# Optimization experiments

Hardware: AMD Instinct MI355X
Metric: run time of the kernel (lower is better)

Reference implementation:

```python
import jax, jax.numpy as jnp
import numpy as np

B, L, D_IN = 2, 4096, 512
H, D_K, D_V, D_OUT = 8, 64, 64, 512


def setup_inputs() -> dict:
    key = jax.random.key(0)
    k0, k1, k2, k3, k4 = jax.random.split(key, 5)
    x = jax.random.normal(k0, (B, L, D_IN), dtype=jnp.float32)
    W_q = jax.random.uniform(k1, (H, D_IN, D_K), dtype=jnp.float32)
    W_k = jax.random.uniform(k2, (H, D_IN, D_K), dtype=jnp.float32)
    W_v = jax.random.uniform(k3, (H, D_IN, D_V), dtype=jnp.float32)
    W_o = jax.random.uniform(k4, (H, D_V, D_OUT), dtype=jnp.float32)
    return {"x": x, "W_q": W_q, "W_k": W_k, "W_v": W_v, "W_o": W_o}


def reference(x, W_q, W_k, W_v, W_o):
    # x: (b, l, d_in); projections per head -> (b, h, l, d)
    Q = jnp.einsum('hjk,blj->bhlk', W_q, x)
    K = jnp.einsum('hjk,blj->bhlk', W_k, x)
    V = jnp.einsum('hjv,blj->bhlv', W_v, x)
    # no softmax: pure bilinear attention (Q K^T) V
    scores = jnp.einsum('bhik,bhjk->bhij', Q, K)          # (b, h, l, l)
    values = jnp.einsum('bhqk,bhkv->bhqv', scores, V)     # (b, h, l, d_v)
    return jnp.einsum('hvo,bhlv->blo', W_o, values)       # (b, l, d_out)
```

## Files before the change

kernel.cpp:

```cpp
#include <hip/hip_runtime.h>
#include <cstdint>


#define BDIM 2
#define LDIM 4096
#define DIN 512
#define HDIM 8
#define DK 64
#define DV 64
#define DOUT 512
#define NXTX 256
#define NMID 128
#define SMEM_MAIN 34816

using bf16_t = __bf16;
typedef __bf16 bf16x8 __attribute__((ext_vector_type(8)));
typedef float floatx4 __attribute__((ext_vector_type(4)));

constexpr size_t OFF_XB  = 4096;
constexpr size_t OFF_XT  = OFF_XB  + (size_t)BDIM * LDIM * DIN * 2;
constexpr size_t OFF_WQT = OFF_XT  + (size_t)BDIM * LDIM * DIN * 2;
constexpr size_t OFF_WKT = OFF_WQT + (size_t)HDIM * DK * DIN * 2;
constexpr size_t OFF_WVT = OFF_WKT + (size_t)HDIM * DK * DIN * 2;
constexpr size_t OFF_WOT = OFF_WVT + (size_t)HDIM * DV * DIN * 2;
constexpr size_t OFF_QP  = OFF_WOT + (size_t)HDIM * DOUT * DV * 2;
constexpr size_t OFF_G32 = OFF_QP  + (size_t)BDIM * LDIM * DIN * 2;
constexpr size_t OFF_MP  = OFF_G32 + (size_t)BDIM * DIN * DIN * 4;

__device__ __forceinline__ unsigned short f2bf(float f) {
    unsigned int u = __builtin_bit_cast(unsigned int, f);
    u += 0x7FFFu + ((u >> 16) & 1u);
    return (unsigned short)(u >> 16);
}

__device__ __forceinline__ float bf2f(unsigned short u) {
    unsigned int v = ((unsigned int)u) << 16;
    return __builtin_bit_cast(float, v);
}

__device__ __forceinline__ void gld_lds16(const void* g, void* l) {
    __builtin_amdgcn_global_load_lds(
        (const __attribute__((address_space(1))) void*)g,
        (__attribute__((address_space(3))) void*)l, 16, 0, 0);
}

template <int BM, int BN, int BK, int OUT_MODE>
__device__ __forceinline__ void gemm_tn(char* smem, const bf16_t* A,
                                        const bf16_t* B, void* Cp, int K,
                                        int lda, int ldb, int ldc, int tm,
                                        int tn) {
    constexpr int WM = BM / 2, WN = BN / 2;
    constexpr int FM = WM / 16, FN = WN / 16;
    constexpr int CPR = BK / 8;
    bf16_t* As = (bf16_t*)smem;
    bf16_t* Bs = As + BM * BK;
    const int tid = threadIdx.x;
    const int lane = tid & 63;
    const int wr = (tid >> 7) & 1;
    const int wc = (tid >> 6) & 1;

    A += (size_t)tm * lda;
    B += (size_t)tn * ldb;

    floatx4 acc[FM][FN] = {};

    for (int k0 = 0; k0 < K; k0 += BK) {
#pragma unroll
        for (int i = 0; i < (BM * CPR) / 256; ++i) {
            int c = i * 256 + tid;
            int m = c / CPR, kc = c % CPR;
            gld_lds16(A + (size_t)m * lda + k0 + kc * 8, As + c * 8);
        }
#pragma unroll
        for (int i = 0; i < (BN * CPR) / 256; ++i) {
            int c = i * 256 + tid;
            int m = c / CPR, kc = c % CPR;
            gld_lds16(B + (size_t)m * ldb + k0 + kc * 8, Bs + c * 8);
        }
        __syncthreads();

#pragma unroll
        for (int kk = 0; kk < BK; kk += 32) {
            bf16x8 aF[FM], bF[FN];
#pragma unroll
            for (int fm = 0; fm < FM; ++fm)
                aF[fm] = *(const bf16x8*)(As + (wr * WM + fm * 16 + (lane & 15)) * BK +
                                          kk + (lane >> 4) * 8);
#pragma unroll
            for (int fn = 0; fn < FN; ++fn)
                bF[fn] = *(const bf16x8*)(Bs + (wc * WN + fn * 16 + (lane & 15)) * BK +
                                          kk + (lane >> 4) * 8);
#pragma unroll
            for (int fm = 0; fm < FM; ++fm)
#pragma unroll
                for (int fn = 0; fn < FN; ++fn)
                    acc[fm][fn] = __builtin_amdgcn_mfma_f32_16x16x32_bf16(
                        aF[fm], bF[fn], acc[fm][fn], 0, 0, 0);
        }
        __syncthreads();
    }

    const int cr4 = (lane >> 4) * 4;
    const int cn = lane & 15;
#pragma unroll
    for (int fm = 0; fm < FM; ++fm)
#pragma unroll
        for (int fn = 0; fn < FN; ++fn)
#pragma unroll
            for (int r = 0; r < 4; ++r) {
                int m = tm + wr * WM + fm * 16 + cr4 + r;
                int n = tn + wc * WN + fn * 16 + cn;
                size_t idx = (size_t)m * ldc + n;
                if (OUT_MODE == 1)
                    ((unsigned short*)Cp)[idx] = f2bf(acc[fm][fn][r]);
                else
                    atomicAdd((float*)Cp + idx, acc[fm][fn][r]);
            }
}

__global__ __launch_bounds__(256) void k_prep(
    const float* __restrict__ x, const float* __restrict__ Wq,
    const float* __restrict__ Wk, const float* __restrict__ Wv,
    const float* __restrict__ Wo, char* __restrict__ ws) {
    __shared__ unsigned short T[64][65];
    unsigned short* xb  = (unsigned short*)(ws + OFF_XB);
    unsigned short* xT  = (unsigned short*)(ws + OFF_XT);
    unsigned short* WqT = (unsigned short*)(ws + OFF_WQT);
    unsigned short* WkT = (unsigned short*)(ws + OFF_WKT);
    unsigned short* WvT = (unsigned short*)(ws + OFF_WVT);
    unsigned short* WoT = (unsigned short*)(ws + OFF_WOT);
    float* G32 = (float*)(ws + OFF_G32);

    const int tid = threadIdx.x;
    const int tr = tid >> 4, tc4 = (tid & 15) * 4;
    const int j = blockIdx.x;

    if (j < 1024) {
        const int b = j >> 9, q = j & 511, lt = q >> 3, it = q & 7;
        const float* src = x + (size_t)b * LDIM * DIN + (size_t)lt * 64 * DIN +
                           it * 64;
        unsigned short* d0 = xb + (size_t)b * LDIM * DIN +
                             (size_t)lt * 64 * DIN + it * 64;
        unsigned short* d1 = xT + (size_t)b * DIN * LDIM +
                             (size_t)it * 64 * LDIM + lt * 64;
#pragma unroll
        for (int p = 0; p < 4; ++p) {
            int r = p * 16 + tr;
            float4 v = *(const float4*)(src + (size_t)r * DIN + tc4);
            ushort4 u = make_ushort4(f2bf(v.x), f2bf(v.y), f2bf(v.z), f2bf(v.w));
            *(ushort4*)(d0 + (size_t)r * DIN + tc4) = u;
            T[r][tc4 + 0] = u.x; T[r][tc4 + 1] = u.y;
            T[r][tc4 + 2] = u.z; T[r][tc4 + 3] = u.w;
        }
        __syncthreads();
#pragma unroll
        for (int p = 0; p < 4; ++p) {
            int c = p * 16 + tr;
            ushort4 u = make_ushort4(T[tc4 + 0][c], T[tc4 + 1][c], T[tc4 + 2][c],
                                     T[tc4 + 3][c]);
            *(ushort4*)(d1 + (size_t)c * LDIM + tc4) = u;
        }
        return;
    }
    if (j < 1280) {
        const int q = j - 1024;
        const int t = q & 7, h = (q >> 3) & 7, typ = q >> 6;
        const float* src;
        unsigned short* dst;
        int rows, cols, r0, c0;
        if (typ == 0) { src = Wq + (size_t)h * DIN * DK; dst = WqT + (size_t)h * DK * DIN;
                        rows = DIN; cols = DK; r0 = t * 64; c0 = 0; }
        else if (typ == 1) { src = Wk + (size_t)h * DIN * DK; dst = WkT + (size_t)h * DK * DIN;
                        rows = DIN; cols = DK; r0 = t * 64; c0 = 0; }
        else if (typ == 2) { src = Wv + (size_t)h * DIN * DV; dst = WvT + (size_t)h * DV * DIN;
                        rows = DIN; cols = DV; r0 = t * 64; c0 = 0; }
        else { src = Wo + (size_t)h * DV * DOUT; dst = WoT + (size_t)h * DOUT * DV;
                        rows = DV; cols = DOUT; r0 = 0; c0 = t * 64; }
#pragma unroll
        for (int p = 0; p < 4; ++p) {
            int r = p * 16 + tr;
            float4 v = *(const float4*)(src + (size_t)(r0 + r) * cols + c0 + tc4);
            T[r][tc4 + 0] = f2bf(v.x); T[r][tc4 + 1] = f2bf(v.y);
            T[r][tc4 + 2] = f2bf(v.z); T[r][tc4 + 3] = f2bf(v.w);
        }
        __syncthreads();
#pragma unroll
        for (int p = 0; p < 4; ++p) {
            int c = p * 16 + tr;
            ushort4 u = make_ushort4(T[tc4 + 0][c], T[tc4 + 1][c], T[tc4 + 2][c],
                                     T[tc4 + 3][c]);
            *(ushort4*)(dst + (size_t)(c0 + c) * rows + r0 + tc4) = u;
        }
        return;
    }
    if (j < 1344) {
        float* g = G32 + (size_t)(j - 1280) * 8192 + tid * 32;
        float4 z = make_float4(0.f, 0.f, 0.f, 0.f);
#pragma unroll
        for (int q = 0; q < 8; ++q) *(float4*)(g + q * 4) = z;
        return;
    }
    {
        ((uint4*)ws)[tid] = make_uint4(0u, 0u, 0u, 0u);
    }
}

__device__ void mid_job(int id, char* smem, const bf16_t* WkT,
                        const bf16_t* WvT, const float* G32,
                        unsigned short* Mp) {
    const int tid = threadIdx.x, lane = tid & 63;
    const int wr = (tid >> 7) & 1, wc = (tid >> 6) & 1;
    const int cr4 = (lane >> 4) * 4, cn = lane & 15;
    const int h = id & 7, b = (id >> 3) & 1, jt = id >> 4;
    const int j0 = jt * 64;
    bf16_t* As  = (bf16_t*)smem;
    bf16_t* Bs  = (bf16_t*)(smem + 8192);
    bf16_t* T2s = (bf16_t*)(smem + 16384);
    bf16_t* Vs  = (bf16_t*)(smem + 25600);
    const bf16_t* Ah = WkT + (size_t)h * DK * DIN;
    const bf16_t* Vh = WvT + (size_t)h * DV * DIN;
    const float* Gb = G32 + (size_t)b * DIN * DIN;

    floatx4 accT[2][2] = {};
    for (int k0 = 0; k0 < DIN; k0 += 64) {
#pragma unroll
        for (int i = 0; i < 2; ++i) {
            int c = i * 256 + tid, m = c >> 3, kc = c & 7;
            gld_lds16(Ah + (size_t)m * DIN + k0 + kc * 8, As + c * 8);
        }
#pragma unroll
        for (int i = 0; i < 2; ++i) {
            int c = i * 256 + tid, n = c >> 3, kc = c & 7;
            const float* g = Gb + (size_t)(j0 + n) * DIN + k0 + kc * 8;
            float4 v0 = *(const float4*)g;
            float4 v1 = *(const float4*)(g + 4);
            unsigned short o[8] = {f2bf(v0.x), f2bf(v0.y), f2bf(v0.z),
                                   f2bf(v0.w), f2bf(v1.x), f2bf(v1.y),
                                   f2bf(v1.z), f2bf(v1.w)};
            *(uint4*)((unsigned short*)Bs + (size_t)c * 8) = *(const uint4*)o;
        }
        __syncthreads();
#pragma unroll
        for (int kk = 0; kk < 64; kk += 32) {
            bf16x8 aF[2], bF[2];
#pragma unroll
            for (int f = 0; f < 2; ++f) {
                aF[f] = *(const bf16x8*)(As + (wr * 32 + f * 16 + cn) * 64 + kk +
                                         (lane >> 4) * 8);
                bF[f] = *(const bf16x8*)(Bs + (wc * 32 + f * 16 + cn) * 64 + kk +
                                         (lane >> 4) * 8);
            }
#pragma unroll
            for (int fm = 0; fm < 2; ++fm)
#pragma unroll
                for (int fn = 0; fn < 2; ++fn)
                    accT[fm][fn] = __builtin_amdgcn_mfma_f32_16x16x32_bf16(
                        aF[fm], bF[fn], accT[fm][fn], 0, 0, 0);
        }
        __syncthreads();
    }
#pragma unroll
    for (int fm = 0; fm < 2; ++fm)
#pragma unroll
        for (int fn = 0; fn < 2; ++fn)
#pragma unroll
            for (int r = 0; r < 4; ++r)
                ((unsigned short*)T2s)[(wr * 32 + fm * 16 + cr4 + r) * 72 +
                                       wc * 32 + fn * 16 + cn] =
                    f2bf(accT[fm][fn][r]);
#pragma unroll
    for (int i = 0; i < 2; ++i) {
        int c = i * 256 + tid, v = c >> 3, kc = c & 7;
        gld_lds16(Vh + (size_t)v * DIN + j0 + kc * 8, Vs + c * 8);
    }
    __syncthreads();

    floatx4 accM[2][2] = {};
#pragma unroll
    for (int kk = 0; kk < 64; kk += 32) {
        bf16x8 aF[2], bF[2];
#pragma unroll
        for (int f = 0; f < 2; ++f) {
            aF[f] = *(const bf16x8*)(T2s + (wr * 32 + f * 16 + cn) * 72 + kk +
                                     (lane >> 4) * 8);
            bF[f] = *(const bf16x8*)(Vs + (wc * 32 + f * 16 + cn) * 64 + kk +
                                     (lane >> 4) * 8);
        }
#pragma unroll
        for (int fm = 0; fm < 2; ++fm)
#pragma unroll
            for (int fn = 0; fn < 2; ++fn)
                accM[fm][fn] = __builtin_amdgcn_mfma_f32_16x16x32_bf16(
                    aF[fm], bF[fn], accM[fm][fn], 0, 0, 0);
    }
    unsigned short* MpD = Mp + ((size_t)((jt * BDIM + b) * HDIM + h)) * (DK * DV);
#pragma unroll
    for (int fm = 0; fm < 2; ++fm)
#pragma unroll
        for (int fn = 0; fn < 2; ++fn)
#pragma unroll
            for (int r = 0; r < 4; ++r)
                MpD[(wr * 32 + fm * 16 + cr4 + r) * 64 + wc * 32 + fn * 16 + cn] =
                    f2bf(accM[fm][fn][r]);
}

__global__ __launch_bounds__(256) void k_main(char* __restrict__ ws) {
    __shared__ __align__(16) char smem[SMEM_MAIN];
    __shared__ int s_old;
    const bf16_t* xb  = (const bf16_t*)(ws + OFF_XB);
    const bf16_t* xT  = (const bf16_t*)(ws + OFF_XT);
    const bf16_t* WqT = (const bf16_t*)(ws + OFF_WQT);
    const bf16_t* WkT = (const bf16_t*)(ws + OFF_WKT);
    const bf16_t* WvT = (const bf16_t*)(ws + OFF_WVT);
    unsigned short* Qp = (unsigned short*)(ws + OFF_QP);
    float* G32 = (float*)(ws + OFF_G32);
    unsigned short* Mp = (unsigned short*)(ws + OFF_MP);
    unsigned* done = (unsigned*)ws;

    const int bid = blockIdx.x;
    const int tid = threadIdx.x;

    if (bid < NXTX) {
        const int b = bid >> 7, r = bid & 127;
        const int ch = r >> 5, t = r & 31;
        const int i0 = (t >> 3) * 128, j0 = (t & 7) * 64;
        const bf16_t* Xb = xT + (size_t)b * DIN * LDIM + ch * 1024;
        gemm_tn<128, 64, 64, 2>(smem, Xb, Xb, G32 + (size_t)b * DIN * DIN, 1024,
                                LDIM, LDIM, DIN, i0, j0);
        __syncthreads();
        if (tid == 0) {
            unsigned old = __hip_atomic_fetch_add(done, 1u, __ATOMIC_RELAXED,
                                                  __HIP_MEMORY_SCOPE_AGENT);
            s_old = (int)old;
        }
        __syncthreads();
        int old = s_old;
        if (old >= NXTX - NMID) {
            if (tid == 0) {
                while (__hip_atomic_load(done, __ATOMIC_RELAXED,
                                         __HIP_MEMORY_SCOPE_AGENT) <
                       (unsigned)NXTX)
                    __builtin_amdgcn_s_sleep(8);
            }
            __syncthreads();
            mid_job(old - (NXTX - NMID), smem, WkT, WvT, G32, Mp);
        }
    } else {
        const int q = bid - NXTX;
        const int b = q >> 7, t = q & 127;
        const int lt = t >> 2, nt = t & 3;
        gemm_tn<128, 128, 64, 1>(smem, xb + (size_t)b * LDIM * DIN, WqT,
                                 Qp + (size_t)b * LDIM * (HDIM * DK), DIN, DIN,
                                 DIN, HDIM * DK, lt * 128, nt * 128);
    }
}

__global__ __launch_bounds__(256) void k_out(const char* __restrict__ ws,
                                             float* __restrict__ out) {
    __shared__ __align__(16) bf16_t Qs[128 * 64];
    __shared__ __align__(16) bf16_t Ws[128 * 64];
    __shared__ __align__(16) bf16_t Ms[64 * 72];
    __shared__ __align__(16) bf16_t PTs[128 * 72];
    const bf16_t* WoT = (const bf16_t*)(ws + OFF_WOT);
    const bf16_t* Qp  = (const bf16_t*)(ws + OFF_QP);
    const unsigned short* Mp = (const unsigned short*)(ws + OFF_MP);

    const int lt = blockIdx.x, nt = blockIdx.y, b = blockIdx.z;
    const int l0 = lt * 128, o0 = nt * 128;
    const int tid = threadIdx.x, lane = tid & 63;
    const int wr = (tid >> 7) & 1, wc = (tid >> 6) & 1;
    const int cr4 = (lane >> 4) * 4, cn = lane & 15;

    floatx4 acc[4][4] = {};

    for (int h = 0; h < HDIM; ++h) {
        {
            const int dk = tid >> 2, v0 = (tid & 3) * 16;
            float s[16] = {0.f, 0.f, 0.f, 0.f, 0.f, 0.f, 0.f, 0.f,
                           0.f, 0.f, 0.f, 0.f, 0.f, 0.f, 0.f, 0.f};
#pragma unroll
            for (int p = 0; p < 8; ++p) {
                const unsigned short* mp =
                    Mp + ((size_t)((p * BDIM + b) * HDIM + h)) * (DK * DV) +
                    dk * 64 + v0;
                uint4 u0 = *(const uint4*)mp;
                uint4 u1 = *(const uint4*)(mp + 8);
                const unsigned short* e0 = (const unsigned short*)&u0;
                const unsigned short* e1 = (const unsigned short*)&u1;
#pragma unroll
                for (int q = 0; q < 8; ++q) {
                    s[q] += bf2f(e0[q]);
                    s[8 + q] += bf2f(e1[q]);
                }
            }
            unsigned short o[16];
#pragma unroll
            for (int q = 0; q < 16; ++q) o[q] = f2bf(s[q]);
            unsigned short* d = (unsigned short*)Ms + dk * 72 + v0;
            *(uint4*)d = *(const uint4*)o;
            *(uint4*)(d + 8) = *(const uint4*)(o + 8);
        }
#pragma unroll
        for (int i = 0; i < 4; ++i) {
            int c = i * 256 + tid, m = c >> 3, kc = c & 7;
            gld_lds16(WoT + ((size_t)h * DOUT + o0 + m) * DV + kc * 8,
                      Ws + c * 8);
            gld_lds16(Qp + (size_t)b * LDIM * 512 + (size_t)(l0 + m) * 512 +
                          h * 64 + kc * 8,
                      Qs + c * 8);
        }
        __syncthreads();

        floatx4 accP[2][4] = {};
#pragma unroll
        for (int kk = 0; kk < 64; kk += 32) {
            bf16x8 aF[2], bF[4];
#pragma unroll
            for (int f = 0; f < 2; ++f)
                aF[f] = *(const bf16x8*)(Ms + (wr * 32 + f * 16 + cn) * 72 + kk +
                                         (lane >> 4) * 8);
#pragma unroll
            for (int f = 0; f < 4; ++f)
                bF[f] = *(const bf16x8*)(Ws + (wc * 64 + f * 16 + cn) * 64 + kk +
                                         (lane >> 4) * 8);
#pragma unroll
            for (int fm = 0; fm < 2; ++fm)
#pragma unroll
                for (int fn = 0; fn < 4; ++fn)
                    accP[fm][fn] = __builtin_amdgcn_mfma_f32_16x16x32_bf16(
                        aF[fm], bF[fn], accP[fm][fn], 0, 0, 0);
        }
#pragma unroll
        for (int fm = 0; fm < 2; ++fm)
#pragma unroll
            for (int fn = 0; fn < 4; ++fn)
#pragma unroll
                for (int r = 0; r < 4; ++r)
                    ((unsigned short*)PTs)[(wc * 64 + fn * 16 + cn) * 72 +
                                           wr * 32 + fm * 16 + cr4 + r] =
                        f2bf(accP[fm][fn][r]);
        __syncthreads();

#pragma unroll
        for (int kk = 0; kk < 64; kk += 32) {
            bf16x8 aF[4], bF[4];
#pragma unroll
            for (int f = 0; f < 4; ++f) {
                aF[f] = *(const bf16x8*)(Qs + (wr * 64 + f * 16 + cn) * 64 + kk +
                                         (lane >> 4) * 8);
                bF[f] = *(const bf16x8*)(PTs + (wc * 64 + f * 16 + cn) * 72 + kk +
                                         (lane >> 4) * 8);
            }
#pragma unroll
            for (int fm = 0; fm < 4; ++fm)
#pragma unroll
                for (int fn = 0; fn < 4; ++fn)
                    acc[fm][fn] = __builtin_amdgcn_mfma_f32_16x16x32_bf16(
                        aF[fm], bF[fn], acc[fm][fn], 0, 0, 0);
        }
        __syncthreads();
    }

    float* ob = out + (size_t)b * LDIM * DOUT;
#pragma unroll
    for (int fm = 0; fm < 4; ++fm)
#pragma unroll
        for (int fn = 0; fn < 4; ++fn)
#pragma unroll
            for (int r = 0; r < 4; ++r) {
                int m = l0 + wr * 64 + fm * 16 + cr4 + r;
                int n = o0 + wc * 64 + fn * 16 + cn;
                ob[(size_t)m * DOUT + n] = acc[fm][fn][r];
            }
}

extern "C" void kernel_launch(void* const* d_in, const int* in_sizes, int n_in,
                              void* d_out, int out_size, void* d_ws, size_t ws_size,
                              hipStream_t stream) {
    const float* x  = (const float*)d_in[0];
    const float* Wq = (const float*)d_in[1];
    const float* Wk = (const float*)d_in[2];
    const float* Wv = (const float*)d_in[3];
    const float* Wo = (const float*)d_in[4];

    k_prep<<<dim3(1345), 256, 0, stream>>>(x, Wq, Wk, Wv, Wo, (char*)d_ws);
    k_main<<<dim3(512), 256, 0, stream>>>((char*)d_ws);
    k_out<<<dim3(32, 4, BDIM), 256, 0, stream>>>((const char*)d_ws,
                                                 (float*)d_out);
}
```

Before: 151.3 us.

## Fuse prep into main kernel with grid barrier and chunked bf16 Gram partials

Merges the conversion/transpose prep kernel into the main kernel using a persistent 512-block grid with a software grid barrier on a monotonic global counter, removing one launch and the G32 zeroing pass. The X^T X Gram matrix is no longer accumulated with fp32 atomics; each K-chunk writes its own bf16 partial tile, and the mid stage sums the four partials when loading. This trades atomic traffic for extra partial reads and bf16 rounding of partials, and relies on all 512 blocks being co-resident for the spin barrier.

```diff
diff --git a/kernel.cpp b/kernel.cpp
--- a/kernel.cpp
+++ b/kernel.cpp
@@ -9,23 +9,26 @@
 #define DK 64
 #define DV 64
 #define DOUT 512
+#define NBLKF 512
 #define NXTX 256
 #define NMID 128
-#define SMEM_MAIN 34816
+#define NCH 4
 
 using bf16_t = __bf16;
 typedef __bf16 bf16x8 __attribute__((ext_vector_type(8)));
 typedef float floatx4 __attribute__((ext_vector_type(4)));
 
-constexpr size_t OFF_XB  = 4096;
+constexpr size_t OFF_XB  = 0;
 constexpr size_t OFF_XT  = OFF_XB  + (size_t)BDIM * LDIM * DIN * 2;
 constexpr size_t OFF_WQT = OFF_XT  + (size_t)BDIM * LDIM * DIN * 2;
 constexpr size_t OFF_WKT = OFF_WQT + (size_t)HDIM * DK * DIN * 2;
 constexpr size_t OFF_WVT = OFF_WKT + (size_t)HDIM * DK * DIN * 2;
 constexpr size_t OFF_WOT = OFF_WVT + (size_t)HDIM * DV * DIN * 2;
 constexpr size_t OFF_QP  = OFF_WOT + (size_t)HDIM * DOUT * DV * 2;
-constexpr size_t OFF_G32 = OFF_QP  + (size_t)BDIM * LDIM * DIN * 2;
-constexpr size_t OFF_MP  = OFF_G32 + (size_t)BDIM * DIN * DIN * 4;
+constexpr size_t OFF_GP  = OFF_QP  + (size_t)BDIM * LDIM * DIN * 2;
+constexpr size_t OFF_MP  = OFF_GP  + (size_t)NCH * BDIM * DIN * DIN * 2;
+
+__device__ unsigned g_ctr[2];
 
 __device__ __forceinline__ unsigned short f2bf(float f) {
     unsigned int u = __builtin_bit_cast(unsigned int, f);
@@ -44,11 +47,24 @@
         (__attribute__((address_space(3))) void*)l, 16, 0, 0);
 }
 
-template <int BM, int BN, int BK, int OUT_MODE>
+__device__ __forceinline__ void st_agent64(unsigned short* p, ushort4 u) {
+    unsigned long long v = (unsigned long long)u.x |
+                           ((unsigned long long)u.y << 16) |
+                           ((unsigned long long)u.z << 32) |
+                           ((unsigned long long)u.w << 48);
+    __hip_atomic_store((unsigned long long*)p, v, __ATOMIC_RELAXED,
+                       __HIP_MEMORY_SCOPE_AGENT);
+}
+__device__ __forceinline__ void st_agent32(unsigned short* p, unsigned v) {
+    __hip_atomic_store((unsigned*)p, v, __ATOMIC_RELAXED,
+                       __HIP_MEMORY_SCOPE_AGENT);
+}
+
+template <int BM, int BN, int BK>
 __device__ __forceinline__ void gemm_tn(char* smem, const bf16_t* A,
-                                        const bf16_t* B, void* Cp, int K,
-                                        int lda, int ldb, int ldc, int tm,
-                                        int tn) {
+                                        const bf16_t* B, unsigned short* Cp,
+                                        int K, int lda, int ldb, int ldc,
+                                        int tm, int tn) {
     constexpr int WM = BM / 2, WN = BN / 2;
     constexpr int FM = WM / 16, FN = WN / 16;
     constexpr int CPR = BK / 8;
@@ -110,103 +126,77 @@
             for (int r = 0; r < 4; ++r) {
                 int m = tm + wr * WM + fm * 16 + cr4 + r;
                 int n = tn + wc * WN + fn * 16 + cn;
-                size_t idx = (size_t)m * ldc + n;
-                if (OUT_MODE == 1)
-                    ((unsigned short*)Cp)[idx] = f2bf(acc[fm][fn][r]);
-                else
-                    atomicAdd((float*)Cp + idx, acc[fm][fn][r]);
-            }
-}
-
-__global__ __launch_bounds__(256) void k_prep(
-    const float* __restrict__ x, const float* __restrict__ Wq,
-    const float* __restrict__ Wk, const float* __restrict__ Wv,
-    const float* __restrict__ Wo, char* __restrict__ ws) {
-    __shared__ unsigned short T[64][65];
-    unsigned short* xb  = (unsigned short*)(ws + OFF_XB);
-    unsigned short* xT  = (unsigned short*)(ws + OFF_XT);
-    unsigned short* WqT = (unsigned short*)(ws + OFF_WQT);
-    unsigned short* WkT = (unsigned short*)(ws + OFF_WKT);
-    unsigned short* WvT = (unsigned short*)(ws + OFF_WVT);
-    unsigned short* WoT = (unsigned short*)(ws + OFF_WOT);
-    float* G32 = (float*)(ws + OFF_G32);
-
-    const int tid = threadIdx.x;
-    const int tr = tid >> 4, tc4 = (tid & 15) * 4;
-    const int j = blockIdx.x;
-
-    if (j < 1024) {
-        const int b = j >> 9, q = j & 511, lt = q >> 3, it = q & 7;
-        const float* src = x + (size_t)b * LDIM * DIN + (size_t)lt * 64 * DIN +
-                           it * 64;
-        unsigned short* d0 = xb + (size_t)b * LDIM * DIN +
-                             (size_t)lt * 64 * DIN + it * 64;
-        unsigned short* d1 = xT + (size_t)b * DIN * LDIM +
-                             (size_t)it * 64 * LDIM + lt * 64;
-#pragma unroll
-        for (int p = 0; p < 4; ++p) {
-            int r = p * 16 + tr;
-            float4 v = *(const float4*)(src + (size_t)r * DIN + tc4);
-            ushort4 u = make_ushort4(f2bf(v.x), f2bf(v.y), f2bf(v.z), f2bf(v.w));
-            *(ushort4*)(d0 + (size_t)r * DIN + tc4) = u;
-            T[r][tc4 + 0] = u.x; T[r][tc4 + 1] = u.y;
-            T[r][tc4 + 2] = u.z; T[r][tc4 + 3] = u.w;
-        }
-        __syncthreads();
-#pragma unroll
-        for (int p = 0; p < 4; ++p) {
-            int c = p * 16 + tr;
-            ushort4 u = make_ushort4(T[tc4 + 0][c], T[tc4 + 1][c], T[tc4 + 2][c],
-                                     T[tc4 + 3][c]);
-            *(ushort4*)(d1 + (size_t)c * LDIM + tc4) = u;
-        }
-        return;
-    }
-    if (j < 1280) {
-        const int q = j - 1024;
-        const int t = q & 7, h = (q >> 3) & 7, typ = q >> 6;
-        const float* src;
-        unsigned short* dst;
-        int rows, cols, r0, c0;
-        if (typ == 0) { src = Wq + (size_t)h * DIN * DK; dst = WqT + (size_t)h * DK * DIN;
-                        rows = DIN; cols = DK; r0 = t * 64; c0 = 0; }
-        else if (typ == 1) { src = Wk + (size_t)h * DIN * DK; dst = WkT + (size_t)h * DK * DIN;
-                        rows = DIN; cols = DK; r0 = t * 64; c0 = 0; }
-        else if (typ == 2) { src = Wv + (size_t)h * DIN * DV; dst = WvT + (size_t)h * DV * DIN;
-                        rows = DIN; cols = DV; r0 = t * 64; c0 = 0; }
-        else { src = Wo + (size_t)h * DV * DOUT; dst = WoT + (size_t)h * DOUT * DV;
-                        rows = DV; cols = DOUT; r0 = 0; c0 = t * 64; }
-#pragma unroll
-        for (int p = 0; p < 4; ++p) {
-            int r = p * 16 + tr;
-            float4 v = *(const float4*)(src + (size_t)(r0 + r) * cols + c0 + tc4);
-            T[r][tc4 + 0] = f2bf(v.x); T[r][tc4 + 1] = f2bf(v.y);
-            T[r][tc4 + 2] = f2bf(v.z); T[r][tc4 + 3] = f2bf(v.w);
-        }
-        __syncthreads();
-#pragma unroll
-        for (int p = 0; p < 4; ++p) {
-            int c = p * 16 + tr;
-            ushort4 u = make_ushort4(T[tc4 + 0][c], T[tc4 + 1][c], T[tc4 + 2][c],
-                                     T[tc4 + 3][c]);
-            *(ushort4*)(dst + (size_t)(c0 + c) * rows + r0 + tc4) = u;
-        }
-        return;
-    }
-    if (j < 1344) {
-        float* g = G32 + (size_t)(j - 1280) * 8192 + tid * 32;
-        float4 z = make_float4(0.f, 0.f, 0.f, 0.f);
-#pragma unroll
-        for (int q = 0; q < 8; ++q) *(float4*)(g + q * 4) = z;
-        return;
-    }
-    {
-        ((uint4*)ws)[tid] = make_uint4(0u, 0u, 0u, 0u);
-    }
+                Cp[(size_t)m * ldc + n] = f2bf(acc[fm][fn][r]);
+            }
+}
+
+__device__ void xtx_job(int bid, char* smem, const bf16_t* xT,
+                        unsigned short* GpB) {
+    const int tid = threadIdx.x, lane = tid & 63;
+    const int wr = (tid >> 7) & 1, wc = (tid >> 6) & 1;
+    const int cr4 = (lane >> 4) * 4, cn = lane & 15;
+    const int b = bid >> 7, r = bid & 127;
+    const int ch = r >> 5, t = r & 31;
+    const int i0 = (t >> 3) * 128, j0 = (t & 7) * 64;
+    bf16_t* As = (bf16_t*)smem;
+    bf16_t* Bs = As + 128 * 64;
+    const bf16_t* Ag = xT + (size_t)b * DIN * LDIM + ch * 1024 +
+                       (size_t)i0 * LDIM;
+    const bf16_t* Bg = xT + (size_t)b * DIN * LDIM + ch * 1024 +
+                       (size_t)j0 * LDIM;
+
+    floatx4 acc[4][2] = {};
+    for (int k0 = 0; k0 < 1024; k0 += 64) {
+#pragma unroll
+        for (int i = 0; i < 4; ++i) {
+            int c = i * 256 + tid, m = c >> 3, kc = c & 7;
+            gld_lds16(Ag + (size_t)m * LDIM + k0 + kc * 8, As + c * 8);
+        }
+#pragma unroll
+        for (int i = 0; i < 2; ++i) {
+            int c = i * 256 + tid, m = c >> 3, kc = c & 7;
+            gld_lds16(Bg + (size_t)m * LDIM + k0 + kc * 8, Bs + c * 8);
+        }
+        __syncthreads();
+#pragma unroll
+        for (int kk = 0; kk < 64; kk += 32) {
+            bf16x8 aF[4], bF[2];
+#pragma unroll
+            for (int fm = 0; fm < 4; ++fm)
+                aF[fm] = *(const bf16x8*)(As + (wr * 64 + fm * 16 + cn) * 64 +
+                                          kk + (lane >> 4) * 8);
+#pragma unroll
+            for (int fn = 0; fn < 2; ++fn)
+                bF[fn] = *(const bf16x8*)(Bs + (wc * 32 + fn * 16 + cn) * 64 +
+                                          kk + (lane >> 4) * 8);
+#pragma unroll
+            for (int fm = 0; fm < 4; ++fm)
+#pragma unroll
+                for (int fn = 0; fn < 2; ++fn)
+                    acc[fm][fn] = __builtin_amdgcn_mfma_f32_16x16x32_bf16(
+                        aF[fm], bF[fn], acc[fm][fn], 0, 0, 0);
+        }
+        __syncthreads();
+    }
+
+    unsigned short* Gt = GpB + (size_t)(ch * 2 + b) * DIN * DIN;
+#pragma unroll
+    for (int fm = 0; fm < 4; ++fm)
+#pragma unroll
+        for (int fn = 0; fn < 2; ++fn) {
+            int m = i0 + wr * 64 + fm * 16 + cr4;
+            int n = j0 + wc * 32 + fn * 16 + cn;
+            unsigned a01 = (unsigned)f2bf(acc[fm][fn][0]) |
+                           ((unsigned)f2bf(acc[fm][fn][1]) << 16);
+            unsigned a23 = (unsigned)f2bf(acc[fm][fn][2]) |
+                           ((unsigned)f2bf(acc[fm][fn][3]) << 16);
+            st_agent32(Gt + (size_t)n * DIN + m, a01);
+            st_agent32(Gt + (size_t)n * DIN + m + 2, a23);
+        }
 }
 
 __device__ void mid_job(int id, char* smem, const bf16_t* WkT,
-                        const bf16_t* WvT, const float* G32,
+                        const bf16_t* WvT, const unsigned short* GpB,
                         unsigned short* Mp) {
     const int tid = threadIdx.x, lane = tid & 63;
     const int wr = (tid >> 7) & 1, wc = (tid >> 6) & 1;
@@ -219,7 +209,6 @@
     bf16_t* Vs  = (bf16_t*)(smem + 25600);
     const bf16_t* Ah = WkT + (size_t)h * DK * DIN;
     const bf16_t* Vh = WvT + (size_t)h * DV * DIN;
-    const float* Gb = G32 + (size_t)b * DIN * DIN;
 
     floatx4 accT[2][2] = {};
     for (int k0 = 0; k0 < DIN; k0 += 64) {
@@ -231,12 +220,19 @@
 #pragma unroll
         for (int i = 0; i < 2; ++i) {
             int c = i * 256 + tid, n = c >> 3, kc = c & 7;
-            const float* g = Gb + (size_t)(j0 + n) * DIN + k0 + kc * 8;
-            float4 v0 = *(const float4*)g;
-            float4 v1 = *(const float4*)(g + 4);
-            unsigned short o[8] = {f2bf(v0.x), f2bf(v0.y), f2bf(v0.z),
-                                   f2bf(v0.w), f2bf(v1.x), f2bf(v1.y),
-                                   f2bf(v1.z), f2bf(v1.w)};
+            const unsigned short* g = GpB + (size_t)b * DIN * DIN +
+                                      (size_t)(j0 + n) * DIN + k0 + kc * 8;
+            float s[8] = {0.f, 0.f, 0.f, 0.f, 0.f, 0.f, 0.f, 0.f};
+#pragma unroll
+            for (int ch = 0; ch < NCH; ++ch) {
+                uint4 u = *(const uint4*)(g + (size_t)ch * 2 * DIN * DIN);
+                const unsigned short* e = (const unsigned short*)&u;
+#pragma unroll
+                for (int q = 0; q < 8; ++q) s[q] += bf2f(e[q]);
+            }
+            unsigned short o[8];
+#pragma unroll
+            for (int q = 0; q < 8; ++q) o[q] = f2bf(s[q]);
             *(uint4*)((unsigned short*)Bs + (size_t)c * 8) = *(const uint4*)o;
         }
         __syncthreads();
@@ -304,54 +300,134 @@
                     f2bf(accM[fm][fn][r]);
 }
 
-__global__ __launch_bounds__(256) void k_main(char* __restrict__ ws) {
-    __shared__ __align__(16) char smem[SMEM_MAIN];
-    __shared__ int s_old;
-    const bf16_t* xb  = (const bf16_t*)(ws + OFF_XB);
-    const bf16_t* xT  = (const bf16_t*)(ws + OFF_XT);
-    const bf16_t* WqT = (const bf16_t*)(ws + OFF_WQT);
-    const bf16_t* WkT = (const bf16_t*)(ws + OFF_WKT);
-    const bf16_t* WvT = (const bf16_t*)(ws + OFF_WVT);
-    unsigned short* Qp = (unsigned short*)(ws + OFF_QP);
-    float* G32 = (float*)(ws + OFF_G32);
-    unsigned short* Mp = (unsigned short*)(ws + OFF_MP);
-    unsigned* done = (unsigned*)ws;
+__global__ __launch_bounds__(256) void k_fused(
+    const float* __restrict__ x, const float* __restrict__ Wq,
+    const float* __restrict__ Wk, const float* __restrict__ Wv,
+    const float* __restrict__ Wo, char* __restrict__ ws) {
+    __shared__ __align__(16) char smem[34816];
+    __shared__ unsigned s_rank;
+    unsigned short* xb  = (unsigned short*)(ws + OFF_XB);
+    unsigned short* xT  = (unsigned short*)(ws + OFF_XT);
+    unsigned short* WqT = (unsigned short*)(ws + OFF_WQT);
+    unsigned short* WkT = (unsigned short*)(ws + OFF_WKT);
+    unsigned short* WvT = (unsigned short*)(ws + OFF_WVT);
+    unsigned short* WoT = (unsigned short*)(ws + OFF_WOT);
+    unsigned short* Qp  = (unsigned short*)(ws + OFF_QP);
+    unsigned short* GpB = (unsigned short*)(ws + OFF_GP);
+    unsigned short* Mp  = (unsigned short*)(ws + OFF_MP);
 
     const int bid = blockIdx.x;
     const int tid = threadIdx.x;
 
+    {
+        unsigned short (*T)[65] = (unsigned short (*)[65])smem;
+        const int tr = tid >> 4, tc4 = (tid & 15) * 4;
+        for (int j = bid; j < 1280; j += NBLKF) {
+            if (j < 1024) {
+                const int b = j >> 9, q = j & 511, lt = q >> 3, it = q & 7;
+                const float* src = x + (size_t)b * LDIM * DIN +
+                                   (size_t)lt * 64 * DIN + it * 64;
+                unsigned short* d0 = xb + (size_t)b * LDIM * DIN +
+                                     (size_t)lt * 64 * DIN + it * 64;
+                unsigned short* d1 = xT + (size_t)b * DIN * LDIM +
+                                     (size_t)it * 64 * LDIM + lt * 64;
+#pragma unroll
+                for (int p = 0; p < 4; ++p) {
+                    int r = p * 16 + tr;
+                    float4 v = *(const float4*)(src + (size_t)r * DIN + tc4);
+                    ushort4 u = make_ushort4(f2bf(v.x), f2bf(v.y), f2bf(v.z),
+                                             f2bf(v.w));
+                    st_agent64(d0 + (size_t)r * DIN + tc4, u);
+                    T[r][tc4 + 0] = u.x; T[r][tc4 + 1] = u.y;
+                    T[r][tc4 + 2] = u.z; T[r][tc4 + 3] = u.w;
+                }
+                __syncthreads();
+#pragma unroll
+                for (int p = 0; p < 4; ++p) {
+                    int c = p * 16 + tr;
+                    ushort4 u = make_ushort4(T[tc4 + 0][c], T[tc4 + 1][c],
+                                             T[tc4 + 2][c], T[tc4 + 3][c]);
+                    st_agent64(d1 + (size_t)c * LDIM + tc4, u);
+                }
+                __syncthreads();
+            } else {
+                const int q = j - 1024;
+                const int t = q & 7, h = (q >> 3) & 7, typ = q >> 6;
+                const float* src;
+                unsigned short* dst;
+                int rows, cols, r0, c0;
+                if (typ == 0) { src = Wq + (size_t)h * DIN * DK;
+                                dst = WqT + (size_t)h * DK * DIN;
+                                rows = DIN; cols = DK; r0 = t * 64; c0 = 0; }
+                else if (typ == 1) { src = Wk + (size_t)h * DIN * DK;
+                                dst = WkT + (size_t)h * DK * DIN;
+                                rows = DIN; cols = DK; r0 = t * 64; c0 = 0; }
+                else if (typ == 2) { src = Wv + (size_t)h * DIN * DV;
+                                dst = WvT + (size_t)h * DV * DIN;
+                                rows = DIN; cols = DV; r0 = t * 64; c0 = 0; }
+                else { src = Wo + (size_t)h * DV * DOUT;
+                                dst = WoT + (size_t)h * DOUT * DV;
+                                rows = DV; cols = DOUT; r0 = 0; c0 = t * 64; }
+#pragma unroll
+                for (int p = 0; p < 4; ++p) {
+                    int r = p * 16 + tr;
+                    float4 v = *(const float4*)(src + (size_t)(r0 + r) * cols +
+                                                c0 + tc4);
+                    T[r][tc4 + 0] = f2bf(v.x); T[r][tc4 + 1] = f2bf(v.y);
+                    T[r][tc4 + 2] = f2bf(v.z); T[r][tc4 + 3] = f2bf(v.w);
+                }
+                __syncthreads();
+#pragma unroll
+                for (int p = 0; p < 4; ++p) {
+                    int c = p * 16 + tr;
+                    ushort4 u = make_ushort4(T[tc4 + 0][c], T[tc4 + 1][c],
+                                             T[tc4 + 2][c], T[tc4 + 3][c]);
+                    st_agent64(dst + (size_t)(c0 + c) * rows + r0 + tc4, u);
+                }
+                __syncthreads();
+            }
+        }
+    }
+
+    __syncthreads();
+    if (tid == 0) {
+        unsigned old = __hip_atomic_fetch_add(&g_ctr[0], 1u, __ATOMIC_RELAXED,
+                                              __HIP_MEMORY_SCOPE_AGENT);
+        unsigned tgt = (old | (NBLKF - 1)) + 1;
+        while ((int)(__hip_atomic_load(&g_ctr[0], __ATOMIC_RELAXED,
+                                       __HIP_MEMORY_SCOPE_AGENT) - tgt) < 0)
+            __builtin_amdgcn_s_sleep(16);
+    }
+    __syncthreads();
+
     if (bid < NXTX) {
-        const int b = bid >> 7, r = bid & 127;
-        const int ch = r >> 5, t = r & 31;
-        const int i0 = (t >> 3) * 128, j0 = (t & 7) * 64;
-        const bf16_t* Xb = xT + (size_t)b * DIN * LDIM + ch * 1024;
-        gemm_tn<128, 64, 64, 2>(smem, Xb, Xb, G32 + (size_t)b * DIN * DIN, 1024,
-                                LDIM, LDIM, DIN, i0, j0);
+        xtx_job(bid, smem, (const bf16_t*)xT, GpB);
         __syncthreads();
         if (tid == 0) {
-            unsigned old = __hip_atomic_fetch_add(done, 1u, __ATOMIC_RELAXED,
+            unsigned old = __hip_atomic_fetch_add(&g_ctr[1], 1u,
+                                                  __ATOMIC_RELAXED,
                                                   __HIP_MEMORY_SCOPE_AGENT);
-            s_old = (int)old;
-        }
-        __syncthreads();
-        int old = s_old;
-        if (old >= NXTX - NMID) {
-            if (tid == 0) {
-                while (__hip_atomic_load(done, __ATOMIC_RELAXED,
-                                         __HIP_MEMORY_SCOPE_AGENT) <
-                       (unsigned)NXTX)
+            s_rank = old & (NXTX - 1);
+            if (s_rank >= NXTX - NMID) {
+                unsigned tgt = (old | (NXTX - 1)) + 1;
+                while ((int)(__hip_atomic_load(&g_ctr[1], __ATOMIC_RELAXED,
+                                               __HIP_MEMORY_SCOPE_AGENT) -
+                             tgt) < 0)
                     __builtin_amdgcn_s_sleep(8);
             }
-            __syncthreads();
-            mid_job(old - (NXTX - NMID), smem, WkT, WvT, G32, Mp);
-        }
+        }
+        __syncthreads();
+        if (s_rank >= NXTX - NMID)
+            mid_job((int)s_rank - (NXTX - NMID), smem, (const bf16_t*)WkT,
+                    (const bf16_t*)WvT, GpB, Mp);
     } else {
         const int q = bid - NXTX;
         const int b = q >> 7, t = q & 127;
         const int lt = t >> 2, nt = t & 3;
-        gemm_tn<128, 128, 64, 1>(smem, xb + (size_t)b * LDIM * DIN, WqT,
-                                 Qp + (size_t)b * LDIM * (HDIM * DK), DIN, DIN,
-                                 DIN, HDIM * DK, lt * 128, nt * 128);
+        gemm_tn<128, 128, 64>(smem, (const bf16_t*)xb + (size_t)b * LDIM * DIN,
+                              (const bf16_t*)WqT,
+                              Qp + (size_t)b * LDIM * (HDIM * DK), DIN, DIN,
+                              DIN, HDIM * DK, lt * 128, nt * 128);
     }
 }
 
@@ -483,8 +559,7 @@
     const float* Wv = (const float*)d_in[3];
     const float* Wo = (const float*)d_in[4];
 
-    k_prep<<<dim3(1345), 256, 0, stream>>>(x, Wq, Wk, Wv, Wo, (char*)d_ws);
-    k_main<<<dim3(512), 256, 0, stream>>>((char*)d_ws);
+    k_fused<<<dim3(NBLKF), 256, 0, stream>>>(x, Wq, Wk, Wv, Wo, (char*)d_ws);
     k_out<<<dim3(32, 4, BDIM), 256, 0, stream>>>((const char*)d_ws,
                                                  (float*)d_out);
 }
```

Measured after the change: 170.1 us. 1.12x slower.
